# Kernel optimization log

Hardware: AMD Instinct MI355X
Metric: run time of the kernel (lower is better)

Reference implementation:

```python
import jax, jax.numpy as jnp
import numpy as np

B, L, V, E, H, NH = 64, 256, 30000, 300, 200, 4
ENC = 2 * H
DH = ENC // NH
SCALING = 1000.0   # 1 / test_temperature (eval path of the module)
BUDGET_PCT = 20.0  # self.budget


def setup_inputs() -> dict:
    key = jax.random.key(0)
    ks = jax.random.split(key, 16)
    x = jax.random.randint(ks[0], (B, L), 0, V)
    lengths = jax.random.randint(ks[1], (B,), L // 2, L + 1)
    mask = jnp.arange(L)[None, :] < lengths[:, None]
    z = jax.random.normal(ks[2], (B, L), jnp.float32)
    g = lambda k, sh, sc: jax.random.normal(k, sh, jnp.float32) * sc
    embed_W = g(ks[3], (V, E), 0.1)
    Wi_f = g(ks[4], (E, 4 * H), 0.05); Wh_f = g(ks[5], (H, 4 * H), 0.05); b_f = jnp.zeros((4 * H,), jnp.float32)
    Wi_b = g(ks[6], (E, 4 * H), 0.05); Wh_b = g(ks[7], (H, 4 * H), 0.05); b_b = jnp.zeros((4 * H,), jnp.float32)
    Wk = g(ks[8], (ENC, ENC), 0.05)
    Wv = g(ks[9], (ENC, ENC), 0.05)
    q = g(ks[10], (NH, DH), 0.1)          # learned pooling state pattern per head
    Wo = g(ks[11], (ENC, ENC), 0.05)       # Hopfield output projection
    out_W = g(ks[12], (ENC, 1), 0.05)
    out_b = jnp.zeros((1,), jnp.float32)
    return dict(x=x, z=z, mask=mask, embed_W=embed_W, Wi_f=Wi_f, Wh_f=Wh_f, b_f=b_f,
                Wi_b=Wi_b, Wh_b=Wh_b, b_b=b_b, Wk=Wk, Wv=Wv, q=q, Wo=Wo,
                out_W=out_W, out_b=out_b)


def _lstm_dir(xproj, mask, Wh, reverse):
    # xproj: [B,L,4H] (x @ Wi + b precomputed), torch gate order i,f,g,o
    def step(carry, inp):
        h, c = carry
        xt, mt = inp
        gates = xt + h @ Wh
        i, f, gg, o = jnp.split(gates, 4, axis=-1)
        c_new = jax.nn.sigmoid(f) * c + jax.nn.sigmoid(i) * jnp.tanh(gg)
        h_new = jax.nn.sigmoid(o) * jnp.tanh(c_new)
        mt = mt[:, None]
        h = jnp.where(mt, h_new, h)  # packed-sequence semantics: freeze past length
        c = jnp.where(mt, c_new, c)
        return (h, c), h
    h0 = jnp.zeros((xproj.shape[0], Wh.shape[0]), xproj.dtype)
    _, hs = jax.lax.scan(step, (h0, h0), (xproj.transpose(1, 0, 2), mask.T), reverse=reverse)
    return hs.transpose(1, 0, 2)  # [B,L,H]


def _budget_project(scores, mask, budget):
    # SparseMAP for budget factor (transition=0): project scores onto
    # {p in [0,1]^L : sum p <= budget}, per (sample, head). scores: [B,NH,L]
    NEG = jnp.float32(-1e9)
    s = jnp.where(mask[:, None, :], scores, NEG)
    b = budget[:, None]  # [B,1]
    p0 = jnp.clip(s, 0.0, 1.0)
    need = jnp.sum(p0, -1) > b
    s_sg = jax.lax.stop_gradient(s)

    def body(i, lohi):
        lo, hi = lohi
        mid = 0.5 * (lo + hi)
        val = jnp.sum(jnp.clip(s_sg - mid[..., None], 0.0, 1.0), -1)
        gt = val > b
        return jnp.where(gt, mid, lo), jnp.where(gt, hi, mid)

    lo = jnp.zeros(s.shape[:2], s.dtype)
    hi = jnp.max(jnp.where(mask[:, None, :], s_sg, 0.0), -1) + 1.0
    lo, hi = jax.lax.fori_loop(0, 60, body, (lo, hi))
    tau0 = 0.5 * (lo + hi)
    # differentiable closed-form tau from the active set (implicit grad of projection)
    r = s - tau0[..., None]
    free = (r > 0.0) & (r < 1.0) & mask[:, None, :]
    hi1 = (r >= 1.0) & mask[:, None, :]
    n_free = jnp.sum(free, -1)
    tau = (jnp.sum(jnp.where(free, s, 0.0), -1) + jnp.sum(hi1, -1) - b) / jnp.maximum(n_free, 1)
    tau = jnp.where(n_free > 0, tau, tau0)
    p = jnp.clip(s - tau[..., None], 0.0, 1.0)
    return jnp.where(need[..., None], p, p0)


def reference(x, z, mask, embed_W, Wi_f, Wh_f, b_f, Wi_b, Wh_b, b_b, Wk, Wv, q, Wo, out_W, out_b):
    emb = embed_W[x]  # [B,L,E]; dropout is identity in eval
    hf = _lstm_dir(emb @ Wi_f + b_f, mask, Wh_f, reverse=False)
    hb = _lstm_dir(emb @ Wi_b + b_b, mask, Wh_b, reverse=True)
    h1 = jnp.concatenate([hf, hb], axis=-1)  # [B,L,ENC]
    K = (h1 @ Wk).reshape(B, L, NH, DH)
    Vv = (h1 @ Wv).reshape(B, L, NH, DH)
    scores = SCALING * jnp.einsum('hd,blhd->bhl', q, K)  # [B,NH,L]
    lengths = jnp.sum(mask, -1)
    budget = jnp.round(BUDGET_PCT / 100.0 * lengths).astype(jnp.float32)
    p = _budget_project(scores, mask, budget)  # [B,NH,L] sparse, sum<=budget
    pooled = jnp.einsum('bhl,blhd->bhd', p, Vv).reshape(B, ENC) @ Wo  # [B,ENC]
    y = jax.nn.sigmoid(pooled @ out_W + out_b)  # [B,1]
    zp = jnp.where(mask, jnp.mean(p, axis=1), 0.0)  # [B,L] rationale probs
    return y, zp
```

## Files before the change

kernel.cpp:

```cpp
#include <hip/hip_runtime.h>
#include <math.h>

#define B_      64
#define L_      256
#define V_      30000
#define E_      300
#define H_      200
#define G4_     800
#define ENC_    400
#define NH_     4
#define DH_     100
#define SCALING_ 1000.0f

__device__ __forceinline__ float sigmoidf_(float x) { return 1.0f / (1.0f + expf(-x)); }

__device__ __forceinline__ float blockSum256(float v, float* red) {
    for (int off = 32; off > 0; off >>= 1) v += __shfl_down(v, off);
    __syncthreads();
    if ((threadIdx.x & 63) == 0) red[threadIdx.x >> 6] = v;
    __syncthreads();
    return red[0] + red[1] + red[2] + red[3];
}
__device__ __forceinline__ float blockMax256(float v, float* red) {
    for (int off = 32; off > 0; off >>= 1) v = fmaxf(v, __shfl_down(v, off));
    __syncthreads();
    if ((threadIdx.x & 63) == 0) red[threadIdx.x >> 6] = v;
    __syncthreads();
    return fmaxf(fmaxf(red[0], red[1]), fmaxf(red[2], red[3]));
}

__global__ void k_prep(const void* __restrict__ maskraw, int* __restrict__ lengths,
                       float* __restrict__ budget) {
    int b = blockIdx.x;
    const unsigned char* mb = (const unsigned char*)maskraw;
    bool is_byte = (mb[1] != 0);
    const int* mi = (const int*)maskraw;
    int cnt = 0;
    for (int l = threadIdx.x; l < L_; l += 64) {
        int v = is_byte ? (int)mb[b * L_ + l] : mi[b * L_ + l];
        cnt += (v != 0) ? 1 : 0;
    }
    for (int off = 32; off > 0; off >>= 1) cnt += __shfl_down(cnt, off);
    if (threadIdx.x == 0) {
        lengths[b] = cnt;
        budget[b] = rintf(0.2f * (float)cnt);
    }
}

__global__ void k_w2(const float* __restrict__ Wo, const float* __restrict__ outW,
                     float* __restrict__ w2) {
    int e = blockIdx.x * blockDim.x + threadIdx.x;
    if (e >= ENC_) return;
    float s = 0.0f;
    for (int j = 0; j < ENC_; j++) s = fmaf(Wo[(size_t)e * ENC_ + j], outW[j], s);
    w2[e] = s;
}

__global__ void k_weff(const float* __restrict__ Wk, const float* __restrict__ Wv,
                       const float* __restrict__ q, const float* __restrict__ w2,
                       float* __restrict__ Weff) {
    int idx = blockIdx.x * blockDim.x + threadIdx.x;
    if (idx >= ENC_ * 8) return;
    int e = idx >> 3, c = idx & 7;
    int h = c & 3;
    bool isV = (c >= 4);
    const float* M = isV ? Wv : Wk;
    float s = 0.0f;
    for (int d = 0; d < DH_; d++) {
        float wq = isV ? w2[h * DH_ + d] : q[h * DH_ + d];
        s = fmaf(M[(size_t)e * ENC_ + h * DH_ + d], wq, s);
    }
    Weff[idx] = s;
}

__global__ void k_pack(const float* __restrict__ Wh_f, const float* __restrict__ Wh_b,
                       float* __restrict__ Wp) {
    int idx = blockIdx.x * 256 + threadIdx.x;
    if (idx >= 2 * H_ * H_ * 4) return;
    int dir = idx / (H_ * H_ * 4);
    int r = idx % (H_ * H_ * 4);
    int k = r / (H_ * 4);
    int r2 = r % (H_ * 4);
    int j = r2 >> 2, g = r2 & 3;
    const float* Wh = dir ? Wh_b : Wh_f;
    Wp[idx] = Wh[(size_t)k * G4_ + g * H_ + j];
}

#define GTM 128
#define GTN 64
#define GKC 16
#define SA_LD (GTM + 4)
#define SB_LD (GTN + 4)
__global__ __launch_bounds__(256) void k_gemm_xproj(const int* __restrict__ x,
        const float* __restrict__ embW,
        const float* __restrict__ Wi_f, const float* __restrict__ b_f,
        const float* __restrict__ Wi_b, const float* __restrict__ b_b,
        float* __restrict__ xproj) {
    __shared__ float sA[GKC * SA_LD];
    __shared__ float sB[GKC * SB_LD];
    __shared__ int srow[GTM];
    int tid = threadIdx.x;
    int tm0 = blockIdx.x * GTM;
    int tn0 = blockIdx.y * GTN;
    if (tid < GTM) srow[tid] = x[tm0 + tid];
    __syncthreads();
    int tx = tid & 15, ty = tid >> 4;
    float acc[8][4];
#pragma unroll
    for (int u = 0; u < 8; u++)
#pragma unroll
        for (int v = 0; v < 4; v++) acc[u][v] = 0.0f;

    int mm = tid >> 1, kk8 = (tid & 1) * 8;
    int kkB = tid >> 4, c4 = (tid & 15) * 4;
    int colB = tn0 + c4;
    const float* bbase = (colB < G4_) ? (Wi_f + colB) : (Wi_b + (colB - G4_));

    for (int k0 = 0; k0 < E_; k0 += GKC) {
        const float* arow = embW + (size_t)srow[mm] * E_ + k0 + kk8;
        if (k0 + GKC <= E_) {
            float4 a0 = *(const float4*)(arow);
            float4 a1 = *(const float4*)(arow + 4);
            sA[(kk8 + 0) * SA_LD + mm] = a0.x;
            sA[(kk8 + 1) * SA_LD + mm] = a0.y;
            sA[(kk8 + 2) * SA_LD + mm] = a0.z;
            sA[(kk8 + 3) * SA_LD + mm] = a0.w;
            sA[(kk8 + 4) * SA_LD + mm] = a1.x;
            sA[(kk8 + 5) * SA_LD + mm] = a1.y;
            sA[(kk8 + 6) * SA_LD + mm] = a1.z;
            sA[(kk8 + 7) * SA_LD + mm] = a1.w;
        } else {
#pragma unroll
            for (int i = 0; i < 8; i++) {
                int k = k0 + kk8 + i;
                sA[(kk8 + i) * SA_LD + mm] = (k < E_) ? arow[i] : 0.0f;
            }
        }
        {
            int kB = k0 + kkB;
            float4 bv = make_float4(0.f, 0.f, 0.f, 0.f);
            if (kB < E_) bv = *(const float4*)(bbase + (size_t)kB * G4_);
            *(float4*)&sB[kkB * SB_LD + c4] = bv;
        }
        __syncthreads();
#pragma unroll
        for (int kk2 = 0; kk2 < GKC; kk2++) {
            float4 a0 = *(const float4*)&sA[kk2 * SA_LD + ty * 8];
            float4 a1 = *(const float4*)&sA[kk2 * SA_LD + ty * 8 + 4];
            float4 b0 = *(const float4*)&sB[kk2 * SB_LD + tx * 4];
            float av[8] = {a0.x, a0.y, a0.z, a0.w, a1.x, a1.y, a1.z, a1.w};
            float bv[4] = {b0.x, b0.y, b0.z, b0.w};
#pragma unroll
            for (int u = 0; u < 8; u++)
#pragma unroll
                for (int v = 0; v < 4; v++) acc[u][v] = fmaf(av[u], bv[v], acc[u][v]);
        }
        __syncthreads();
    }
    int col = tn0 + tx * 4;
    float4 bias = (col < G4_) ? *(const float4*)(b_f + col)
                              : *(const float4*)(b_b + (col - G4_));
#pragma unroll
    for (int u = 0; u < 8; u++) {
        int m = tm0 + ty * 8 + u;
        float4 o;
        o.x = acc[u][0] + bias.x;
        o.y = acc[u][1] + bias.y;
        o.z = acc[u][2] + bias.z;
        o.w = acc[u][3] + bias.w;
        *(float4*)&xproj[(size_t)m * 1600 + col] = o;
    }
}

#define KS2 50
__global__ __launch_bounds__(512, 2) void k_lstm(const float* __restrict__ xproj,
        const float4* __restrict__ Wp, const int* __restrict__ lengths,
        float* __restrict__ hf, float* __restrict__ hb,
        unsigned long long* __restrict__ hx) {
    int pid = blockIdx.x;
    int chain = pid & 127;
    int half = pid >> 7;
    int partner = pid ^ 128;
    int b = chain >> 1, dir = chain & 1;
    int jbase = half * 100;
    const float4* W = Wp + (size_t)dir * H_ * H_;
    float* hout = dir ? hb : hf;
    int len = lengths[b];
    __shared__ float sh[256];
    __shared__ float4 sPart[4][128];
    __shared__ int scnt;
    int tid = threadIdx.x;
    int q = tid >> 7, j = tid & 127;
    bool act = (j < 100);
    int u = jbase + j;
    bool partnerQ = ((q >> 1) == (half ^ 1));
    int pq0 = (half ^ 1) * 2;

    float4 w[KS2];
    if (act) {
        const float4* wp = W + (size_t)(q * KS2) * H_ + u;
#pragma unroll
        for (int k = 0; k < KS2; k++) w[k] = wp[(size_t)k * H_];
    }
    if (tid < H_) sh[tid] = 0.0f;
    if (tid == 0) scnt = 0;
    float c = 0.0f;
    float hv_prev = 0.0f;
    int t_prev = -1;
    __syncthreads();
    const float* xp = xproj + (size_t)b * L_ * 1600 + dir * G4_;
    const float4* h4 = (const float4*)(sh + q * KS2);
    const float2* h2t = (const float2*)(sh + q * KS2 + 48);

    for (int s = 0; s < len; s++) {
        int t = dir ? (len - 1 - s) : s;
        if (tid < 100 && t_prev >= 0)
            hout[((size_t)b * L_ + t_prev) * H_ + jbase + tid] = hv_prev;
        if (s > 0 && q == pq0 && j < 100) {
            size_t idx = ((size_t)(((s - 1) & 1) * 256 + partner)) * 128 + j;
            unsigned long long got;
            do {
                got = __hip_atomic_load(&hx[idx], __ATOMIC_RELAXED,
                                        __HIP_MEMORY_SCOPE_AGENT);
            } while ((unsigned)(got >> 32) != (unsigned)s);
            sh[(half ^ 1) * 100 + j] = __uint_as_float((unsigned)got);
            __threadfence_block();
            __hip_atomic_fetch_add(&scnt, 1, __ATOMIC_RELAXED,
                                   __HIP_MEMORY_SCOPE_WORKGROUP);
        }
        if (act) {
            if (partnerQ && s > 0) {
                int target = 100 * s;
                while (__hip_atomic_load(&scnt, __ATOMIC_RELAXED,
                                         __HIP_MEMORY_SCOPE_WORKGROUP) < target) {}
            }
            float xv = xp[(size_t)t * 1600 + q * H_ + u];
            float4 acc = make_float4(0.f, 0.f, 0.f, 0.f);
#pragma unroll
            for (int k4 = 0; k4 < 12; k4++) {
                float4 hk = h4[k4];
                const float4 w0 = w[k4 * 4 + 0], w1 = w[k4 * 4 + 1];
                const float4 w2 = w[k4 * 4 + 2], w3 = w[k4 * 4 + 3];
                acc.x = fmaf(hk.x, w0.x, acc.x); acc.y = fmaf(hk.x, w0.y, acc.y);
                acc.z = fmaf(hk.x, w0.z, acc.z); acc.w = fmaf(hk.x, w0.w, acc.w);
                acc.x = fmaf(hk.y, w1.x, acc.x); acc.y = fmaf(hk.y, w1.y, acc.y);
                acc.z = fmaf(hk.y, w1.z, acc.z); acc.w = fmaf(hk.y, w1.w, acc.w);
                acc.x = fmaf(hk.z, w2.x, acc.x); acc.y = fmaf(hk.z, w2.y, acc.y);
                acc.z = fmaf(hk.z, w2.z, acc.z); acc.w = fmaf(hk.z, w2.w, acc.w);
                acc.x = fmaf(hk.w, w3.x, acc.x); acc.y = fmaf(hk.w, w3.y, acc.y);
                acc.z = fmaf(hk.w, w3.z, acc.z); acc.w = fmaf(hk.w, w3.w, acc.w);
            }
            {
                float2 ht = *h2t;
                const float4 w0 = w[48], w1 = w[49];
                acc.x = fmaf(ht.x, w0.x, acc.x); acc.y = fmaf(ht.x, w0.y, acc.y);
                acc.z = fmaf(ht.x, w0.z, acc.z); acc.w = fmaf(ht.x, w0.w, acc.w);
                acc.x = fmaf(ht.y, w1.x, acc.x); acc.y = fmaf(ht.y, w1.y, acc.y);
                acc.z = fmaf(ht.y, w1.z, acc.z); acc.w = fmaf(ht.y, w1.w, acc.w);
            }
            if (q == 0) acc.x += xv;
            else if (q == 1) acc.y += xv;
            else if (q == 2) acc.z += xv;
            else acc.w += xv;
            sPart[q][j] = acc;
        }
        __syncthreads();
        if (tid < 100) {
            float4 p0 = sPart[0][tid], p1 = sPart[1][tid];
            float4 p2 = sPart[2][tid], p3 = sPart[3][tid];
            float ai = p0.x + p1.x + p2.x + p3.x;
            float af = p0.y + p1.y + p2.y + p3.y;
            float ag = p0.z + p1.z + p2.z + p3.z;
            float ao = p0.w + p1.w + p2.w + p3.w;
            float ii = sigmoidf_(ai), ff = sigmoidf_(af);
            float gg = tanhf(ag), oo = sigmoidf_(ao);
            c = ff * c + ii * gg;
            float hv = oo * tanhf(c);
            sh[jbase + tid] = hv;
            unsigned long long pk = ((unsigned long long)(unsigned)(s + 1) << 32)
                                  | (unsigned long long)__float_as_uint(hv);
            __hip_atomic_store(&hx[((size_t)((s & 1) * 256 + pid)) * 128 + tid], pk,
                               __ATOMIC_RELAXED, __HIP_MEMORY_SCOPE_AGENT);
            hv_prev = hv; t_prev = t;
        }
        __syncthreads();
    }
    if (tid < 100 && t_prev >= 0)
        hout[((size_t)b * L_ + t_prev) * H_ + jbase + tid] = hv_prev;
    for (int i = tid; i < (L_ - len) * 100; i += 512) {
        int t = len + i / 100, uu = jbase + i % 100;
        hout[((size_t)b * L_ + t) * H_ + uu] = dir ? 0.0f : sh[uu];
    }
}

__global__ __launch_bounds__(256) void k_proj(const float* __restrict__ hf,
        const float* __restrict__ hb, const float* __restrict__ Weff,
        float* __restrict__ scores, float* __restrict__ vproj) {
    __shared__ float sW[ENC_ * 8];
    int tid = threadIdx.x;
    for (int i = tid; i < ENC_ * 8; i += 256) sW[i] = Weff[i];
    __syncthreads();
    int pos = blockIdx.x * 32 + (tid >> 3);
    int o = tid & 7;
    int b = pos >> 8, l = pos & 255;
    const float* hfr = hf + (size_t)pos * H_;
    const float* hbr = hb + (size_t)pos * H_;
    float s = 0.0f;
#pragma unroll 4
    for (int e = 0; e < H_; e++) s = fmaf(hfr[e], sW[e * 8 + o], s);
#pragma unroll 4
    for (int e = 0; e < H_; e++) s = fmaf(hbr[e], sW[(H_ + e) * 8 + o], s);
    if (o < NH_) scores[((size_t)b * NH_ + o) * L_ + l] = SCALING_ * s;
    else        vproj[(size_t)pos * NH_ + (o - NH_)] = s;
}

__global__ __launch_bounds__(256) void k_budget(const float* __restrict__ scores,
        const int* __restrict__ lengths, const float* __restrict__ budget,
        float* __restrict__ p) {
    __shared__ float red[4];
    int bh = blockIdx.x;
    int b = bh >> 2;
    int l = threadIdx.x;
    int len = lengths[b];
    float bud = budget[b];
    bool m = (l < len);
    float s = m ? scores[(size_t)bh * L_ + l] : -1.0e9f;
    float p0 = fminf(fmaxf(s, 0.0f), 1.0f);
    float sum_p0 = blockSum256(p0, red);
    bool need = (sum_p0 > bud);
    float hi = blockMax256(m ? s : 0.0f, red) + 1.0f;
    float lo = 0.0f;
    for (int it = 0; it < 60; it++) {
        float mid = 0.5f * (lo + hi);
        float val = blockSum256(fminf(fmaxf(s - mid, 0.0f), 1.0f), red);
        if (val > bud) lo = mid; else hi = mid;
    }
    float tau0 = 0.5f * (lo + hi);
    float r = s - tau0;
    bool fr  = (r > 0.0f) && (r < 1.0f) && m;
    bool h1f = (r >= 1.0f) && m;
    float n_free   = blockSum256(fr ? 1.0f : 0.0f, red);
    float sum_free = blockSum256(fr ? s : 0.0f, red);
    float n_hi     = blockSum256(h1f ? 1.0f : 0.0f, red);
    float tau = (sum_free + n_hi - bud) / fmaxf(n_free, 1.0f);
    tau = (n_free > 0.0f) ? tau : tau0;
    float pv = fminf(fmaxf(s - tau, 0.0f), 1.0f);
    p[(size_t)bh * L_ + l] = need ? pv : p0;
}

__global__ __launch_bounds__(256) void k_final(const float* __restrict__ p,
        const float* __restrict__ vproj, const int* __restrict__ lengths,
        const float* __restrict__ out_b, float* __restrict__ dout) {
    __shared__ float red[4];
    int b = blockIdx.x;
    int l = threadIdx.x;
    int len = lengths[b];
    float p0 = p[((size_t)b * NH_ + 0) * L_ + l];
    float p1 = p[((size_t)b * NH_ + 1) * L_ + l];
    float p2 = p[((size_t)b * NH_ + 2) * L_ + l];
    float p3 = p[((size_t)b * NH_ + 3) * L_ + l];
    dout[B_ + (size_t)b * L_ + l] = (l < len) ? 0.25f * (p0 + p1 + p2 + p3) : 0.0f;
    const float* vp = vproj + ((size_t)b * L_ + l) * NH_;
    float contrib = p0 * vp[0] + p1 * vp[1] + p2 * vp[2] + p3 * vp[3];
    float tot = blockSum256(contrib, red);
    if (l == 0) dout[b] = 1.0f / (1.0f + expf(-(tot + out_b[0])));
}

extern "C" void kernel_launch(void* const* d_in, const int* in_sizes, int n_in,
                              void* d_out, int out_size, void* d_ws, size_t ws_size,
                              hipStream_t stream) {
    const int*   x    = (const int*)d_in[0];
    const void*  mask = d_in[2];
    const float* embW = (const float*)d_in[3];
    const float* Wi_f = (const float*)d_in[4];
    const float* Wh_f = (const float*)d_in[5];
    const float* b_f  = (const float*)d_in[6];
    const float* Wi_b = (const float*)d_in[7];
    const float* Wh_b = (const float*)d_in[8];
    const float* b_b  = (const float*)d_in[9];
    const float* Wk   = (const float*)d_in[10];
    const float* Wv   = (const float*)d_in[11];
    const float* q    = (const float*)d_in[12];
    const float* Wo   = (const float*)d_in[13];
    const float* outW = (const float*)d_in[14];
    const float* outb = (const float*)d_in[15];
    float* dout = (float*)d_out;

    float* ws     = (float*)d_ws;
    float* xproj  = ws;
    float* hf     = xproj + (size_t)16384 * 1600;
    float* hb     = hf + (size_t)16384 * 200;
    float* scores = hb + (size_t)16384 * 200;
    float* vproj  = scores + 65536;
    float* p      = vproj + 65536;
    float* Weff   = p + 65536;
    float* w2     = Weff + 3200;
    float* budget = w2 + 400;
    int*   lengths= (int*)(budget + 64);
    float* Wp     = (float*)(lengths + 64);

    unsigned long long* hx64 = (unsigned long long*)vproj;

    k_prep<<<B_, 64, 0, stream>>>(mask, lengths, budget);
    k_w2<<<2, 256, 0, stream>>>(Wo, outW, w2);
    k_weff<<<13, 256, 0, stream>>>(Wk, Wv, q, w2, Weff);
    k_pack<<<(2 * H_ * H_ * 4 + 255) / 256, 256, 0, stream>>>(Wh_f, Wh_b, Wp);
    k_gemm_xproj<<<dim3(16384 / GTM, 1600 / GTN), 256, 0, stream>>>(x, embW, Wi_f, b_f, Wi_b, b_b, xproj);

    {
        const float4* Wp4 = (const float4*)Wp;
        void* args[] = { (void*)&xproj, (void*)&Wp4, (void*)&lengths,
                         (void*)&hf, (void*)&hb, (void*)&hx64 };
        hipLaunchCooperativeKernel((const void*)k_lstm, dim3(256), dim3(512),
                                   args, 0, stream);
    }

    k_proj<<<(B_ * L_) / 32, 256, 0, stream>>>(hf, hb, Weff, scores, vproj);
    k_budget<<<B_ * NH_, 256, 0, stream>>>(scores, lengths, budget, p);
    k_final<<<B_, 256, 0, stream>>>(p, vproj, lengths, outb, dout);
}
```

Baseline: 900.6 us.

## Add fast single-slot h exchange with sc0 polling alongside double-buffered fallback

The LSTM's two cooperating workgroups per chain now publish each new hidden value to a single-slot buffer with a volatile store and to the existing double-buffered slot. The poller first reads the single slot with an inline global_load using sc0 and falls back to the agent-scope atomic load. The xproj load is hoisted before the spin-wait, and the hout store is moved after the poll for one half. The aim is to cut per-timestep cross-workgroup handoff latency on the serial recurrence. The cost is reliance on cache-coherence behaviour of the sc0 load, and two buffers now alias the scores and p workspace.

```diff
diff --git a/kernel.cpp b/kernel.cpp
--- a/kernel.cpp
+++ b/kernel.cpp
@@ -176,7 +176,8 @@
 __global__ __launch_bounds__(512, 2) void k_lstm(const float* __restrict__ xproj,
         const float4* __restrict__ Wp, const int* __restrict__ lengths,
         float* __restrict__ hf, float* __restrict__ hb,
-        unsigned long long* __restrict__ hx) {
+        unsigned long long* __restrict__ hxS,
+        unsigned long long* __restrict__ hxF) {
     int pid = blockIdx.x;
     int chain = pid & 127;
     int half = pid >> 7;
@@ -195,6 +196,7 @@
     int u = jbase + j;
     bool partnerQ = ((q >> 1) == (half ^ 1));
     int pq0 = (half ^ 1) * 2;
+    bool pollerLane = (q == pq0) && (j < 100);
 
     float4 w[KS2];
     if (act) {
@@ -214,27 +216,37 @@
 
     for (int s = 0; s < len; s++) {
         int t = dir ? (len - 1 - s) : s;
-        if (tid < 100 && t_prev >= 0)
+        if (t_prev >= 0 && tid < 100 && pq0 != 0)
             hout[((size_t)b * L_ + t_prev) * H_ + jbase + tid] = hv_prev;
-        if (s > 0 && q == pq0 && j < 100) {
-            size_t idx = ((size_t)(((s - 1) & 1) * 256 + partner)) * 128 + j;
+        float xv = 0.0f;
+        if (act) xv = xp[(size_t)t * 1600 + q * H_ + u];
+        if (s > 0 && pollerLane) {
+            size_t fidx = (size_t)partner * 128 + j;
+            size_t sidx = ((size_t)(((s - 1) & 1) * 256 + partner)) * 128 + j;
+            const unsigned long long* fap = hxF + fidx;
             unsigned long long got;
-            do {
-                got = __hip_atomic_load(&hx[idx], __ATOMIC_RELAXED,
+            for (;;) {
+                asm volatile("global_load_dwordx2 %0, %1, off sc0\n\t"
+                             "s_waitcnt vmcnt(0)"
+                             : "=v"(got) : "v"(fap) : "memory");
+                if ((unsigned)(got >> 32) == (unsigned)s) break;
+                got = __hip_atomic_load(&hxS[sidx], __ATOMIC_RELAXED,
                                         __HIP_MEMORY_SCOPE_AGENT);
-            } while ((unsigned)(got >> 32) != (unsigned)s);
+                if ((unsigned)(got >> 32) == (unsigned)s) break;
+            }
             sh[(half ^ 1) * 100 + j] = __uint_as_float((unsigned)got);
             __threadfence_block();
             __hip_atomic_fetch_add(&scnt, 1, __ATOMIC_RELAXED,
                                    __HIP_MEMORY_SCOPE_WORKGROUP);
         }
+        if (t_prev >= 0 && tid < 100 && pq0 == 0)
+            hout[((size_t)b * L_ + t_prev) * H_ + jbase + tid] = hv_prev;
         if (act) {
             if (partnerQ && s > 0) {
                 int target = 100 * s;
                 while (__hip_atomic_load(&scnt, __ATOMIC_RELAXED,
                                          __HIP_MEMORY_SCOPE_WORKGROUP) < target) {}
             }
-            float xv = xp[(size_t)t * 1600 + q * H_ + u];
             float4 acc = make_float4(0.f, 0.f, 0.f, 0.f);
 #pragma unroll
             for (int k4 = 0; k4 < 12; k4++) {
@@ -279,7 +291,8 @@
             sh[jbase + tid] = hv;
             unsigned long long pk = ((unsigned long long)(unsigned)(s + 1) << 32)
                                   | (unsigned long long)__float_as_uint(hv);
-            __hip_atomic_store(&hx[((size_t)((s & 1) * 256 + pid)) * 128 + tid], pk,
+            *(volatile unsigned long long*)(hxF + (size_t)pid * 128 + tid) = pk;
+            __hip_atomic_store(&hxS[((size_t)((s & 1) * 256 + pid)) * 128 + tid], pk,
                                __ATOMIC_RELAXED, __HIP_MEMORY_SCOPE_AGENT);
             hv_prev = hv; t_prev = t;
         }
@@ -399,7 +412,8 @@
     int*   lengths= (int*)(budget + 64);
     float* Wp     = (float*)(lengths + 64);
 
-    unsigned long long* hx64 = (unsigned long long*)vproj;
+    unsigned long long* hxS = (unsigned long long*)scores;
+    unsigned long long* hxF = (unsigned long long*)p;
 
     k_prep<<<B_, 64, 0, stream>>>(mask, lengths, budget);
     k_w2<<<2, 256, 0, stream>>>(Wo, outW, w2);
@@ -410,7 +424,7 @@
     {
         const float4* Wp4 = (const float4*)Wp;
         void* args[] = { (void*)&xproj, (void*)&Wp4, (void*)&lengths,
-                         (void*)&hf, (void*)&hb, (void*)&hx64 };
+                         (void*)&hf, (void*)&hb, (void*)&hxS, (void*)&hxF };
         hipLaunchCooperativeKernel((const void*)k_lstm, dim3(256), dim3(512),
                                    args, 0, stream);
     }
```

Measured after the change: 1.025 ms. +13.8%, slower.

## Interleave two batch chains per LSTM block to hide cross-block exchange latency

Applied to the files above, without the earlier changes.

Each LSTM workgroup now advances two independent sequences (adjacent batch items, same direction) in alternation, halving the cooperative grid from 256 to 128 blocks. While one chain waits for its partner block's half of the hidden state, the other chain's matvec and gate work runs, so the global-memory polling latency of the split-hidden exchange can overlap with useful compute. The exchange buffer grows to hold both chains and moves to the scores region. The trade-off is twice the serial work per block and half the CUs in use, and each timestep now runs to the longer of the two sequence lengths.

```diff
diff --git a/kernel.cpp b/kernel.cpp
--- a/kernel.cpp
+++ b/kernel.cpp
@@ -173,28 +173,67 @@
 }
 
 #define KS2 50
+__device__ __forceinline__ float4 matvec200(const float* __restrict__ shc,
+                                            const float4* __restrict__ w,
+                                            int q, float xv) {
+    const float4* h4 = (const float4*)(shc + q * KS2);
+    const float2* h2t = (const float2*)(shc + q * KS2 + 48);
+    float4 acc = make_float4(0.f, 0.f, 0.f, 0.f);
+#pragma unroll
+    for (int k4 = 0; k4 < 12; k4++) {
+        float4 hk = h4[k4];
+        const float4 w0 = w[k4 * 4 + 0], w1 = w[k4 * 4 + 1];
+        const float4 w2 = w[k4 * 4 + 2], w3 = w[k4 * 4 + 3];
+        acc.x = fmaf(hk.x, w0.x, acc.x); acc.y = fmaf(hk.x, w0.y, acc.y);
+        acc.z = fmaf(hk.x, w0.z, acc.z); acc.w = fmaf(hk.x, w0.w, acc.w);
+        acc.x = fmaf(hk.y, w1.x, acc.x); acc.y = fmaf(hk.y, w1.y, acc.y);
+        acc.z = fmaf(hk.y, w1.z, acc.z); acc.w = fmaf(hk.y, w1.w, acc.w);
+        acc.x = fmaf(hk.z, w2.x, acc.x); acc.y = fmaf(hk.z, w2.y, acc.y);
+        acc.z = fmaf(hk.z, w2.z, acc.z); acc.w = fmaf(hk.z, w2.w, acc.w);
+        acc.x = fmaf(hk.w, w3.x, acc.x); acc.y = fmaf(hk.w, w3.y, acc.y);
+        acc.z = fmaf(hk.w, w3.z, acc.z); acc.w = fmaf(hk.w, w3.w, acc.w);
+    }
+    {
+        float2 ht = *h2t;
+        const float4 w0 = w[48], w1 = w[49];
+        acc.x = fmaf(ht.x, w0.x, acc.x); acc.y = fmaf(ht.x, w0.y, acc.y);
+        acc.z = fmaf(ht.x, w0.z, acc.z); acc.w = fmaf(ht.x, w0.w, acc.w);
+        acc.x = fmaf(ht.y, w1.x, acc.x); acc.y = fmaf(ht.y, w1.y, acc.y);
+        acc.z = fmaf(ht.y, w1.z, acc.z); acc.w = fmaf(ht.y, w1.w, acc.w);
+    }
+    if (q == 0) acc.x += xv;
+    else if (q == 1) acc.y += xv;
+    else if (q == 2) acc.z += xv;
+    else acc.w += xv;
+    return acc;
+}
+
 __global__ __launch_bounds__(512, 2) void k_lstm(const float* __restrict__ xproj,
         const float4* __restrict__ Wp, const int* __restrict__ lengths,
         float* __restrict__ hf, float* __restrict__ hb,
         unsigned long long* __restrict__ hx) {
     int pid = blockIdx.x;
-    int chain = pid & 127;
-    int half = pid >> 7;
-    int partner = pid ^ 128;
-    int b = chain >> 1, dir = chain & 1;
+    int pg = pid & 63;
+    int half = pid >> 6;
+    int partner = pid ^ 64;
+    int dir = pg & 1;
+    int b0 = (pg >> 1) * 2;
+    int b1 = b0 + 1;
     int jbase = half * 100;
     const float4* W = Wp + (size_t)dir * H_ * H_;
     float* hout = dir ? hb : hf;
-    int len = lengths[b];
-    __shared__ float sh[256];
+    int lenA = lengths[b0], lenB = lengths[b1];
+    int smax = lenA > lenB ? lenA : lenB;
+    __shared__ float sh[2][256];
     __shared__ float4 sPart[4][128];
-    __shared__ int scnt;
+    __shared__ int scnt[2];
     int tid = threadIdx.x;
     int q = tid >> 7, j = tid & 127;
     bool act = (j < 100);
     int u = jbase + j;
     bool partnerQ = ((q >> 1) == (half ^ 1));
     int pq0 = (half ^ 1) * 2;
+    bool pollerLane = (q == pq0) && (j < 100);
 
     float4 w[KS2];
     if (act) {
@@ -202,94 +241,124 @@
 #pragma unroll
         for (int k = 0; k < KS2; k++) w[k] = wp[(size_t)k * H_];
     }
-    if (tid < H_) sh[tid] = 0.0f;
-    if (tid == 0) scnt = 0;
-    float c = 0.0f;
-    float hv_prev = 0.0f;
-    int t_prev = -1;
-    __syncthreads();
-    const float* xp = xproj + (size_t)b * L_ * 1600 + dir * G4_;
-    const float4* h4 = (const float4*)(sh + q * KS2);
-    const float2* h2t = (const float2*)(sh + q * KS2 + 48);
-
-    for (int s = 0; s < len; s++) {
-        int t = dir ? (len - 1 - s) : s;
-        if (tid < 100 && t_prev >= 0)
-            hout[((size_t)b * L_ + t_prev) * H_ + jbase + tid] = hv_prev;
-        if (s > 0 && q == pq0 && j < 100) {
-            size_t idx = ((size_t)(((s - 1) & 1) * 256 + partner)) * 128 + j;
-            unsigned long long got;
-            do {
-                got = __hip_atomic_load(&hx[idx], __ATOMIC_RELAXED,
-                                        __HIP_MEMORY_SCOPE_AGENT);
-            } while ((unsigned)(got >> 32) != (unsigned)s);
-            sh[(half ^ 1) * 100 + j] = __uint_as_float((unsigned)got);
-            __threadfence_block();
-            __hip_atomic_fetch_add(&scnt, 1, __ATOMIC_RELAXED,
-                                   __HIP_MEMORY_SCOPE_WORKGROUP);
-        }
-        if (act) {
-            if (partnerQ && s > 0) {
-                int target = 100 * s;
-                while (__hip_atomic_load(&scnt, __ATOMIC_RELAXED,
-                                         __HIP_MEMORY_SCOPE_WORKGROUP) < target) {}
-            }
-            float xv = xp[(size_t)t * 1600 + q * H_ + u];
-            float4 acc = make_float4(0.f, 0.f, 0.f, 0.f);
-#pragma unroll
-            for (int k4 = 0; k4 < 12; k4++) {
-                float4 hk = h4[k4];
-                const float4 w0 = w[k4 * 4 + 0], w1 = w[k4 * 4 + 1];
-                const float4 w2 = w[k4 * 4 + 2], w3 = w[k4 * 4 + 3];
-                acc.x = fmaf(hk.x, w0.x, acc.x); acc.y = fmaf(hk.x, w0.y, acc.y);
-                acc.z = fmaf(hk.x, w0.z, acc.z); acc.w = fmaf(hk.x, w0.w, acc.w);
-                acc.x = fmaf(hk.y, w1.x, acc.x); acc.y = fmaf(hk.y, w1.y, acc.y);
-                acc.z = fmaf(hk.y, w1.z, acc.z); acc.w = fmaf(hk.y, w1.w, acc.w);
-                acc.x = fmaf(hk.z, w2.x, acc.x); acc.y = fmaf(hk.z, w2.y, acc.y);
-                acc.z = fmaf(hk.z, w2.z, acc.z); acc.w = fmaf(hk.z, w2.w, acc.w);
-                acc.x = fmaf(hk.w, w3.x, acc.x); acc.y = fmaf(hk.w, w3.y, acc.y);
-                acc.z = fmaf(hk.w, w3.z, acc.z); acc.w = fmaf(hk.w, w3.w, acc.w);
-            }
-            {
-                float2 ht = *h2t;
-                const float4 w0 = w[48], w1 = w[49];
-                acc.x = fmaf(ht.x, w0.x, acc.x); acc.y = fmaf(ht.x, w0.y, acc.y);
-                acc.z = fmaf(ht.x, w0.z, acc.z); acc.w = fmaf(ht.x, w0.w, acc.w);
-                acc.x = fmaf(ht.y, w1.x, acc.x); acc.y = fmaf(ht.y, w1.y, acc.y);
-                acc.z = fmaf(ht.y, w1.z, acc.z); acc.w = fmaf(ht.y, w1.w, acc.w);
-            }
-            if (q == 0) acc.x += xv;
-            else if (q == 1) acc.y += xv;
-            else if (q == 2) acc.z += xv;
-            else acc.w += xv;
-            sPart[q][j] = acc;
-        }
-        __syncthreads();
-        if (tid < 100) {
-            float4 p0 = sPart[0][tid], p1 = sPart[1][tid];
-            float4 p2 = sPart[2][tid], p3 = sPart[3][tid];
-            float ai = p0.x + p1.x + p2.x + p3.x;
-            float af = p0.y + p1.y + p2.y + p3.y;
-            float ag = p0.z + p1.z + p2.z + p3.z;
-            float ao = p0.w + p1.w + p2.w + p3.w;
-            float ii = sigmoidf_(ai), ff = sigmoidf_(af);
-            float gg = tanhf(ag), oo = sigmoidf_(ao);
-            c = ff * c + ii * gg;
-            float hv = oo * tanhf(c);
-            sh[jbase + tid] = hv;
-            unsigned long long pk = ((unsigned long long)(unsigned)(s + 1) << 32)
-                                  | (unsigned long long)__float_as_uint(hv);
-            __hip_atomic_store(&hx[((size_t)((s & 1) * 256 + pid)) * 128 + tid], pk,
-                               __ATOMIC_RELAXED, __HIP_MEMORY_SCOPE_AGENT);
-            hv_prev = hv; t_prev = t;
-        }
-        __syncthreads();
-    }
-    if (tid < 100 && t_prev >= 0)
-        hout[((size_t)b * L_ + t_prev) * H_ + jbase + tid] = hv_prev;
-    for (int i = tid; i < (L_ - len) * 100; i += 512) {
-        int t = len + i / 100, uu = jbase + i % 100;
-        hout[((size_t)b * L_ + t) * H_ + uu] = dir ? 0.0f : sh[uu];
+    if (tid < 256) { sh[0][tid] = 0.0f; sh[1][tid] = 0.0f; }
+    if (tid < 2) scnt[tid] = 0;
+    float cA = 0.0f, cB = 0.0f;
+    float hvA = 0.0f, hvB = 0.0f;
+    int tA = -1, tB = -1;
+    __syncthreads();
+    const float* xpA = xproj + (size_t)b0 * L_ * 1600 + dir * G4_;
+    const float* xpB = xproj + (size_t)b1 * L_ * 1600 + dir * G4_;
+
+    for (int s = 0; s < smax; s++) {
+        if (tid < 100 && tB >= 0) {
+            hout[((size_t)b1 * L_ + tB) * H_ + jbase + tid] = hvB;
+            tB = -1;
+        }
+        if (s < lenA) {
+            int t = dir ? (lenA - 1 - s) : s;
+            if (s > 0 && pollerLane) {
+                size_t sidx = ((size_t)((((s - 1) & 1) * 2 + 0) * 128 + partner)) * 128 + j;
+                unsigned long long got;
+                do {
+                    got = __hip_atomic_load(&hx[sidx], __ATOMIC_RELAXED,
+                                            __HIP_MEMORY_SCOPE_AGENT);
+                } while ((unsigned)(got >> 32) != (unsigned)s);
+                sh[0][(half ^ 1) * 100 + j] = __uint_as_float((unsigned)got);
+                __threadfence_block();
+                __hip_atomic_fetch_add(&scnt[0], 1, __ATOMIC_RELAXED,
+                                       __HIP_MEMORY_SCOPE_WORKGROUP);
+            }
+            if (act) {
+                if (partnerQ && s > 0) {
+                    int target = 100 * s;
+                    while (__hip_atomic_load(&scnt[0], __ATOMIC_RELAXED,
+                                             __HIP_MEMORY_SCOPE_WORKGROUP) < target) {}
+                }
+                float xv = xpA[(size_t)t * 1600 + q * H_ + u];
+                sPart[q][j] = matvec200(sh[0], w, q, xv);
+            }
+            __syncthreads();
+            if (tid < 100) {
+                float4 p0 = sPart[0][tid], p1 = sPart[1][tid];
+                float4 p2 = sPart[2][tid], p3 = sPart[3][tid];
+                float ai = p0.x + p1.x + p2.x + p3.x;
+                float af = p0.y + p1.y + p2.y + p3.y;
+                float ag = p0.z + p1.z + p2.z + p3.z;
+                float ao = p0.w + p1.w + p2.w + p3.w;
+                float ii = sigmoidf_(ai), ff = sigmoidf_(af);
+                float gg = tanhf(ag), oo = sigmoidf_(ao);
+                cA = ff * cA + ii * gg;
+                float hv = oo * tanhf(cA);
+                sh[0][jbase + tid] = hv;
+                unsigned long long pk = ((unsigned long long)(unsigned)(s + 1) << 32)
+                                      | (unsigned long long)__float_as_uint(hv);
+                __hip_atomic_store(&hx[((size_t)(((s & 1) * 2 + 0) * 128 + pid)) * 128 + tid],
+                                   pk, __ATOMIC_RELAXED, __HIP_MEMORY_SCOPE_AGENT);
+                hvA = hv; tA = t;
+            }
+            __syncthreads();
+        }
+        if (tid < 100 && tA >= 0) {
+            hout[((size_t)b0 * L_ + tA) * H_ + jbase + tid] = hvA;
+            tA = -1;
+        }
+        if (s < lenB) {
+            int t = dir ? (lenB - 1 - s) : s;
+            if (s > 0 && pollerLane) {
+                size_t sidx = ((size_t)((((s - 1) & 1) * 2 + 1) * 128 + partner)) * 128 + j;
+                unsigned long long got;
+                do {
+                    got = __hip_atomic_load(&hx[sidx], __ATOMIC_RELAXED,
+                                            __HIP_MEMORY_SCOPE_AGENT);
+                } while ((unsigned)(got >> 32) != (unsigned)s);
+                sh[1][(half ^ 1) * 100 + j] = __uint_as_float((unsigned)got);
+                __threadfence_block();
+                __hip_atomic_fetch_add(&scnt[1], 1, __ATOMIC_RELAXED,
+                                       __HIP_MEMORY_SCOPE_WORKGROUP);
+            }
+            if (act) {
+                if (partnerQ && s > 0) {
+                    int target = 100 * s;
+                    while (__hip_atomic_load(&scnt[1], __ATOMIC_RELAXED,
+                                             __HIP_MEMORY_SCOPE_WORKGROUP) < target) {}
+                }
+                float xv = xpB[(size_t)t * 1600 + q * H_ + u];
+                sPart[q][j] = matvec200(sh[1], w, q, xv);
+            }
+            __syncthreads();
+            if (tid < 100) {
+                float4 p0 = sPart[0][tid], p1 = sPart[1][tid];
+                float4 p2 = sPart[2][tid], p3 = sPart[3][tid];
+                float ai = p0.x + p1.x + p2.x + p3.x;
+                float af = p0.y + p1.y + p2.y + p3.y;
+                float ag = p0.z + p1.z + p2.z + p3.z;
+                float ao = p0.w + p1.w + p2.w + p3.w;
+                float ii = sigmoidf_(ai), ff = sigmoidf_(af);
+                float gg = tanhf(ag), oo = sigmoidf_(ao);
+                cB = ff * cB + ii * gg;
+                float hv = oo * tanhf(cB);
+                sh[1][jbase + tid] = hv;
+                unsigned long long pk = ((unsigned long long)(unsigned)(s + 1) << 32)
+                                      | (unsigned long long)__float_as_uint(hv);
+                __hip_atomic_store(&hx[((size_t)(((s & 1) * 2 + 1) * 128 + pid)) * 128 + tid],
+                                   pk, __ATOMIC_RELAXED, __HIP_MEMORY_SCOPE_AGENT);
+                hvB = hv; tB = t;
+            }
+            __syncthreads();
+        }
+    }
+    if (tid < 100) {
+        if (tA >= 0) hout[((size_t)b0 * L_ + tA) * H_ + jbase + tid] = hvA;
+        if (tB >= 0) hout[((size_t)b1 * L_ + tB) * H_ + jbase + tid] = hvB;
+    }
+    for (int i = tid; i < (L_ - lenA) * 100; i += 512) {
+        int t = lenA + i / 100, uu = jbase + i % 100;
+        hout[((size_t)b0 * L_ + t) * H_ + uu] = dir ? 0.0f : sh[0][uu];
+    }
+    for (int i = tid; i < (L_ - lenB) * 100; i += 512) {
+        int t = lenB + i / 100, uu = jbase + i % 100;
+        hout[((size_t)b1 * L_ + t) * H_ + uu] = dir ? 0.0f : sh[1][uu];
     }
 }
 
@@ -399,7 +468,7 @@
     int*   lengths= (int*)(budget + 64);
     float* Wp     = (float*)(lengths + 64);
 
-    unsigned long long* hx64 = (unsigned long long*)vproj;
+    unsigned long long* hx = (unsigned long long*)scores;
 
     k_prep<<<B_, 64, 0, stream>>>(mask, lengths, budget);
     k_w2<<<2, 256, 0, stream>>>(Wo, outW, w2);
@@ -410,8 +479,8 @@
     {
         const float4* Wp4 = (const float4*)Wp;
         void* args[] = { (void*)&xproj, (void*)&Wp4, (void*)&lengths,
-                         (void*)&hf, (void*)&hb, (void*)&hx64 };
-        hipLaunchCooperativeKernel((const void*)k_lstm, dim3(256), dim3(512),
+                         (void*)&hf, (void*)&hb, (void*)&hx };
+        hipLaunchCooperativeKernel((const void*)k_lstm, dim3(128), dim3(512),
                                    args, 0, stream);
     }
 
```

Measured after the change: 1.341 ms. 1.49x slower.
